# Kernel optimization log

Hardware: AMD Instinct MI355X
Metric: run time of the kernel (lower is better)

Reference implementation:

```python
import jax, jax.numpy as jnp
import numpy as np

B, N, D, C = 256, 256, 512, 1024
EPS = 1e-12  # F.normalize eps


def _l2norm(x):
    n = jnp.linalg.norm(x, axis=-1, keepdims=True)
    return x / jnp.maximum(n, EPS)


def setup_inputs() -> dict:
    key = jax.random.key(0)
    k1, k2, k3 = jax.random.split(key, 3)
    return {
        "image_tokens": jax.random.normal(k1, (B, N, D), dtype=jnp.float32),
        "text_features": jax.random.normal(k2, (C, D), dtype=jnp.float32),
        "log_tau": jnp.asarray(np.log(0.07), dtype=jnp.float32),
        "log_attn_tau": jnp.asarray(np.log(0.07), dtype=jnp.float32),
        "pid_labels": jax.random.randint(k3, (B,), 0, C),
    }


def reference(image_tokens, text_features, log_tau, log_attn_tau, pid_labels):
    toks = _l2norm(image_tokens.astype(jnp.float32))        # [B,N,D]
    txt = _l2norm(text_features.astype(jnp.float32))        # [C,D]
    sims = jnp.einsum('bnd,cd->bnc', toks, txt)             # [B,N,C]
    gt = pid_labels.astype(jnp.int32)
    # sims[arange(B), :, gt] -> [B,N]
    sims_gt = jnp.take_along_axis(sims, gt[:, None, None], axis=2)[..., 0]
    attn_tau = jnp.clip(jnp.exp(log_attn_tau), 0.01, 1.0)
    w = jax.nn.softmax(sims_gt / attn_tau, axis=1)          # [B,N]
    logits = jnp.einsum('bn,bnc->bc', w, sims)              # [B,C]
    tau = jnp.clip(jnp.exp(log_tau), 0.01, 1.0)
    logits = logits / tau
    # cross_entropy with label_smoothing=0.0, mean reduction
    logp = jax.nn.log_softmax(logits, axis=-1)
    nll = -jnp.take_along_axis(logp, gt[:, None], axis=1)[:, 0]
    return jnp.mean(nll)
```

## Files before the change

kernel.cpp:

```cpp
#include <hip/hip_runtime.h>
#include <math.h>

#define Bb 256
#define Nn 256
#define Dd 512
#define Cc 1024
#define KC 8
#define KD (Dd / KC)
#define BT 8

__device__ __forceinline__ float waveReduceSum(float v) {
    #pragma unroll
    for (int off = 32; off > 0; off >>= 1)
        v += __shfl_xor(v, off, 64);
    return v;
}
__device__ __forceinline__ float waveReduceMax(float v) {
    #pragma unroll
    for (int off = 32; off > 0; off >>= 1)
        v = fmaxf(v, __shfl_xor(v, off, 64));
    return v;
}

__global__ void k_txt_prep(const float* __restrict__ txt, float* __restrict__ txt_t) {
    __shared__ float ssp[32][8];
    __shared__ float inv[32];
    __shared__ float tile[32][33];
    const int c0 = blockIdx.x * 32;
    const int t = threadIdx.x;
    {
        const int r = t >> 3, seg = t & 7;
        const float4* p = (const float4*)(txt + (size_t)(c0 + r) * Dd + seg * 64);
        float s = 0.f;
        #pragma unroll
        for (int i = 0; i < 16; ++i) {
            const float4 a = p[i];
            s += a.x*a.x + a.y*a.y + a.z*a.z + a.w*a.w;
        }
        ssp[r][seg] = s;
    }
    __syncthreads();
    if (t < 32) {
        float s = 0.f;
        #pragma unroll
        for (int j = 0; j < 8; ++j) s += ssp[t][j];
        inv[t] = 1.0f / fmaxf(sqrtf(s), 1e-12f);
    }
    __syncthreads();
    const int dx = t & 31, r4 = t >> 5;
    const int dt0 = blockIdx.y * 128;
    for (int dt = dt0; dt < dt0 + 128; dt += 32) {
        #pragma unroll
        for (int rr = r4; rr < 32; rr += 8)
            tile[rr][dx] = txt[(size_t)(c0 + rr) * Dd + dt + dx] * inv[rr];
        __syncthreads();
        #pragma unroll
        for (int rr = r4; rr < 32; rr += 8)
            txt_t[(size_t)(dt + rr) * Cc + c0 + dx] = tile[dx][rr];
        __syncthreads();
    }
}

__global__ void __launch_bounds__(1024) k_attn_q(const float* __restrict__ toks,
                                                 const float* __restrict__ txt,
                                                 const int* __restrict__ pid,
                                                 const float* __restrict__ log_attn_tau,
                                                 float* __restrict__ q) {
    const int b = blockIdx.x;
    const int tid = threadIdx.x;
    const int wv = tid >> 6;
    const int lane = tid & 63;
    __shared__ float xg[Dd];
    __shared__ float r8[8];
    __shared__ float qpart_s[16][Dd];
    __shared__ float ms[16], Ss[16];

    const int g = pid[b];
    float v = 0.f;
    if (tid < Dd) v = txt[(size_t)g * Dd + tid];
    float p = v * v;
    p = waveReduceSum(p);
    if (lane == 0 && wv < 8) r8[wv] = p;
    __syncthreads();
    const float tot = r8[0]+r8[1]+r8[2]+r8[3]+r8[4]+r8[5]+r8[6]+r8[7];
    const float invg = 1.0f / fmaxf(sqrtf(tot), 1e-12f);
    if (tid < Dd) xg[tid] = v * invg;
    __syncthreads();

    float at = expf(log_attn_tau[0]);
    at = fminf(fmaxf(at, 0.01f), 1.0f);
    const float iat = 1.0f / at;

    const float4 xg0 = *(const float4*)&xg[lane * 8];
    const float4 xg1 = *(const float4*)&xg[lane * 8 + 4];

    float m = -INFINITY, S = 0.0f;
    float qa[8] = {0.f, 0.f, 0.f, 0.f, 0.f, 0.f, 0.f, 0.f};

    const float* base = toks + ((size_t)b * Nn + wv * 16) * Dd + (size_t)lane * 8;
    float4 c0[4], c1[4];
    #pragma unroll
    for (int k = 0; k < 4; ++k) {
        c0[k] = *(const float4*)(base + k * Dd);
        c1[k] = *(const float4*)(base + k * Dd + 4);
    }
    #pragma unroll
    for (int batch = 0; batch < 4; ++batch) {
        float4 n0[4], n1[4];
        if (batch < 3) {
            const float* pn = base + (batch + 1) * 4 * Dd;
            #pragma unroll
            for (int k = 0; k < 4; ++k) {
                n0[k] = *(const float4*)(pn + k * Dd);
                n1[k] = *(const float4*)(pn + k * Dd + 4);
            }
        }
        float dt[4], ss[4];
        #pragma unroll
        for (int k = 0; k < 4; ++k) {
            dt[k] = c0[k].x*xg0.x + c0[k].y*xg0.y + c0[k].z*xg0.z + c0[k].w*xg0.w
                  + c1[k].x*xg1.x + c1[k].y*xg1.y + c1[k].z*xg1.z + c1[k].w*xg1.w;
            ss[k] = c0[k].x*c0[k].x + c0[k].y*c0[k].y + c0[k].z*c0[k].z + c0[k].w*c0[k].w
                  + c1[k].x*c1[k].x + c1[k].y*c1[k].y + c1[k].z*c1[k].z + c1[k].w*c1[k].w;
        }
        #pragma unroll
        for (int off = 32; off > 0; off >>= 1) {
            #pragma unroll
            for (int k = 0; k < 4; ++k) {
                dt[k] += __shfl_xor(dt[k], off, 64);
                ss[k] += __shfl_xor(ss[k], off, 64);
            }
        }
        #pragma unroll
        for (int k = 0; k < 4; ++k) {
            const float inv = 1.0f / fmaxf(sqrtf(ss[k]), 1e-12f);
            const float s = dt[k] * inv;
            if (s > m) {
                const float sc = expf((m - s) * iat);
                S = S * sc + 1.0f;
                qa[0] = qa[0]*sc + inv*c0[k].x; qa[1] = qa[1]*sc + inv*c0[k].y;
                qa[2] = qa[2]*sc + inv*c0[k].z; qa[3] = qa[3]*sc + inv*c0[k].w;
                qa[4] = qa[4]*sc + inv*c1[k].x; qa[5] = qa[5]*sc + inv*c1[k].y;
                qa[6] = qa[6]*sc + inv*c1[k].z; qa[7] = qa[7]*sc + inv*c1[k].w;
                m = s;
            } else {
                const float e = expf((s - m) * iat);
                S += e;
                const float w = e * inv;
                qa[0] = fmaf(w, c0[k].x, qa[0]); qa[1] = fmaf(w, c0[k].y, qa[1]);
                qa[2] = fmaf(w, c0[k].z, qa[2]); qa[3] = fmaf(w, c0[k].w, qa[3]);
                qa[4] = fmaf(w, c1[k].x, qa[4]); qa[5] = fmaf(w, c1[k].y, qa[5]);
                qa[6] = fmaf(w, c1[k].z, qa[6]); qa[7] = fmaf(w, c1[k].w, qa[7]);
            }
        }
        #pragma unroll
        for (int k = 0; k < 4; ++k) { c0[k] = n0[k]; c1[k] = n1[k]; }
    }
    #pragma unroll
    for (int j = 0; j < 8; ++j) qpart_s[wv][lane * 8 + j] = qa[j];
    if (lane == 0) { ms[wv] = m; Ss[wv] = S; }
    __syncthreads();
    if (tid < Dd) {
        float M = -INFINITY;
        #pragma unroll
        for (int w = 0; w < 16; ++w) M = fmaxf(M, ms[w]);
        float Stot = 0.f, acc = 0.f;
        #pragma unroll
        for (int w = 0; w < 16; ++w) {
            const float sc = expf((ms[w] - M) * iat);
            Stot = fmaf(Ss[w], sc, Stot);
            acc = fmaf(qpart_s[w][tid], sc, acc);
        }
        q[(size_t)b * Dd + tid] = acc / Stot;
    }
}

__global__ void k_logits(const float* __restrict__ q, const float* __restrict__ txt_t,
                         float* __restrict__ part) {
    const int b0 = blockIdx.x * BT;
    const int kc = blockIdx.y;
    const int d0 = kc * KD;
    const int t = threadIdx.x;
    __shared__ float qs[BT][KD];
    for (int i = t; i < BT * KD; i += 256)
        qs[i >> 6][i & 63] = q[(size_t)(b0 + (i >> 6)) * Dd + d0 + (i & 63)];
    __syncthreads();
    const float4* xt = (const float4*)txt_t;
    float4 a[BT];
    #pragma unroll
    for (int j = 0; j < BT; ++j) a[j] = make_float4(0.f, 0.f, 0.f, 0.f);
    #pragma unroll 2
    for (int d = 0; d < KD; d += 4) {
        const float4 x0 = xt[(size_t)(d0 + d + 0) * (Cc / 4) + t];
        const float4 x1 = xt[(size_t)(d0 + d + 1) * (Cc / 4) + t];
        const float4 x2 = xt[(size_t)(d0 + d + 2) * (Cc / 4) + t];
        const float4 x3 = xt[(size_t)(d0 + d + 3) * (Cc / 4) + t];
        #pragma unroll
        for (int j = 0; j < BT; ++j) {
            const float4 qj = *(const float4*)&qs[j][d];
            a[j].x = fmaf(qj.x,x0.x,a[j].x); a[j].y = fmaf(qj.x,x0.y,a[j].y); a[j].z = fmaf(qj.x,x0.z,a[j].z); a[j].w = fmaf(qj.x,x0.w,a[j].w);
            a[j].x = fmaf(qj.y,x1.x,a[j].x); a[j].y = fmaf(qj.y,x1.y,a[j].y); a[j].z = fmaf(qj.y,x1.z,a[j].z); a[j].w = fmaf(qj.y,x1.w,a[j].w);
            a[j].x = fmaf(qj.z,x2.x,a[j].x); a[j].y = fmaf(qj.z,x2.y,a[j].y); a[j].z = fmaf(qj.z,x2.z,a[j].z); a[j].w = fmaf(qj.z,x2.w,a[j].w);
            a[j].x = fmaf(qj.w,x3.x,a[j].x); a[j].y = fmaf(qj.w,x3.y,a[j].y); a[j].z = fmaf(qj.w,x3.z,a[j].z); a[j].w = fmaf(qj.w,x3.w,a[j].w);
        }
    }
    float* pb = part + ((size_t)kc * Bb + b0) * Cc;
    #pragma unroll
    for (int j = 0; j < BT; ++j) ((float4*)(pb + (size_t)j * Cc))[t] = a[j];
}

__global__ void k_lse(const float* __restrict__ part, const int* __restrict__ pid,
                      const float* __restrict__ log_tau, float* __restrict__ nll) {
    const int b = blockIdx.x;
    const int t = threadIdx.x;
    float4 l = {0,0,0,0};
    #pragma unroll
    for (int kc = 0; kc < KC; ++kc) {
        const float4 p = ((const float4*)(part + ((size_t)kc * Bb + b) * Cc))[t];
        l.x += p.x; l.y += p.y; l.z += p.z; l.w += p.w;
    }
    float tau = expf(log_tau[0]);
    tau = fminf(fmaxf(tau, 0.01f), 1.0f);
    const float itau = 1.0f / tau;
    l.x *= itau; l.y *= itau; l.z *= itau; l.w *= itau;

    const int g = pid[b];
    __shared__ float redm[4], reds[4], sgt;
    if ((g >> 2) == t) {
        const float v[4] = {l.x, l.y, l.z, l.w};
        sgt = v[g & 3];
    }
    float m = fmaxf(fmaxf(l.x, l.y), fmaxf(l.z, l.w));
    m = waveReduceMax(m);
    if ((t & 63) == 0) redm[t >> 6] = m;
    __syncthreads();
    m = fmaxf(fmaxf(redm[0], redm[1]), fmaxf(redm[2], redm[3]));
    float e = expf(l.x - m) + expf(l.y - m) + expf(l.z - m) + expf(l.w - m);
    e = waveReduceSum(e);
    if ((t & 63) == 0) reds[t >> 6] = e;
    __syncthreads();
    if (t == 0) {
        const float S = reds[0] + reds[1] + reds[2] + reds[3];
        nll[b] = m + logf(S) - sgt;
    }
}

__global__ void k_mean(const float* __restrict__ nll, float* __restrict__ out) {
    float v = nll[threadIdx.x];
    __shared__ float red[4];
    v = waveReduceSum(v);
    if ((threadIdx.x & 63) == 0) red[threadIdx.x >> 6] = v;
    __syncthreads();
    if (threadIdx.x == 0) out[0] = (red[0] + red[1] + red[2] + red[3]) * (1.0f / (float)Bb);
}

extern "C" void kernel_launch(void* const* d_in, const int* in_sizes, int n_in,
                              void* d_out, int out_size, void* d_ws, size_t ws_size,
                              hipStream_t stream) {
    const float* toks = (const float*)d_in[0];
    const float* txt = (const float*)d_in[1];
    const float* log_tau = (const float*)d_in[2];
    const float* log_attn_tau = (const float*)d_in[3];
    const int* pid = (const int*)d_in[4];
    float* out = (float*)d_out;

    float* ws = (float*)d_ws;
    float* txt_t = ws;
    float* q     = txt_t + (size_t)Dd * Cc;
    float* part  = q + (size_t)Bb * Dd;
    float* nll   = part + (size_t)KC * Bb * Cc;

    k_txt_prep<<<dim3(Cc / 32, Dd / 128), 256, 0, stream>>>(txt, txt_t);
    k_attn_q<<<Bb, 1024, 0, stream>>>(toks, txt, pid, log_attn_tau, q);
    k_logits<<<dim3(Bb / BT, KC), 256, 0, stream>>>(q, txt_t, part);
    k_lse<<<Bb, 256, 0, stream>>>(part, pid, log_tau, nll);
    k_mean<<<1, 256, 0, stream>>>(nll, out);
}
```

Measured before the change: 219.6 us.

## Fuse text normalization into attention kernel and merge LSE with mean via atomics

Text-feature normalization and transpose move into k_attn_q: each of the 256 blocks normalizes and transposes 4 text rows, which removes the separate k_txt_prep launch. k_lse and k_mean merge into one kernel that accumulates each sample's scaled NLL with atomicAdd, and the last block, found through an atomic counter, writes the result. This saves two kernel launches. In exchange, the transposed stores are uncoalesced, the float sum order becomes nondeterministic, and the accumulators are zeroed inside k_attn_q with a cross-kernel ordering assumption.

New measurement: 220.9 us. No clear change (+0.6%).

```diff
diff --git a/kernel.cpp b/kernel.cpp
--- a/kernel.cpp
+++ b/kernel.cpp
@@ -22,69 +22,50 @@
     return v;
 }
 
-__global__ void k_txt_prep(const float* __restrict__ txt, float* __restrict__ txt_t) {
-    __shared__ float ssp[32][8];
-    __shared__ float inv[32];
-    __shared__ float tile[32][33];
-    const int c0 = blockIdx.x * 32;
-    const int t = threadIdx.x;
-    {
-        const int r = t >> 3, seg = t & 7;
-        const float4* p = (const float4*)(txt + (size_t)(c0 + r) * Dd + seg * 64);
-        float s = 0.f;
-        #pragma unroll
-        for (int i = 0; i < 16; ++i) {
-            const float4 a = p[i];
-            s += a.x*a.x + a.y*a.y + a.z*a.z + a.w*a.w;
-        }
-        ssp[r][seg] = s;
-    }
-    __syncthreads();
-    if (t < 32) {
-        float s = 0.f;
-        #pragma unroll
-        for (int j = 0; j < 8; ++j) s += ssp[t][j];
-        inv[t] = 1.0f / fmaxf(sqrtf(s), 1e-12f);
-    }
-    __syncthreads();
-    const int dx = t & 31, r4 = t >> 5;
-    const int dt0 = blockIdx.y * 128;
-    for (int dt = dt0; dt < dt0 + 128; dt += 32) {
-        #pragma unroll
-        for (int rr = r4; rr < 32; rr += 8)
-            tile[rr][dx] = txt[(size_t)(c0 + rr) * Dd + dt + dx] * inv[rr];
-        __syncthreads();
-        #pragma unroll
-        for (int rr = r4; rr < 32; rr += 8)
-            txt_t[(size_t)(dt + rr) * Cc + c0 + dx] = tile[dx][rr];
-        __syncthreads();
-    }
-}
-
 __global__ void __launch_bounds__(1024) k_attn_q(const float* __restrict__ toks,
                                                  const float* __restrict__ txt,
                                                  const int* __restrict__ pid,
                                                  const float* __restrict__ log_attn_tau,
-                                                 float* __restrict__ q) {
+                                                 float* __restrict__ q,
+                                                 float* __restrict__ txt_t,
+                                                 float* __restrict__ accf,
+                                                 int* __restrict__ cnt) {
     const int b = blockIdx.x;
     const int tid = threadIdx.x;
     const int wv = tid >> 6;
     const int lane = tid & 63;
     __shared__ float xg[Dd];
     __shared__ float r8[8];
+    __shared__ float tss[16];
     __shared__ float qpart_s[16][Dd];
     __shared__ float ms[16], Ss[16];
+
+    if (b == 0 && tid == 0) { accf[0] = 0.0f; cnt[0] = 0; }
 
     const int g = pid[b];
     float v = 0.f;
     if (tid < Dd) v = txt[(size_t)g * Dd + tid];
-    float p = v * v;
-    p = waveReduceSum(p);
-    if (lane == 0 && wv < 8) r8[wv] = p;
-    __syncthreads();
+
+    const int c0 = b * 4;
+    const int row = tid >> 8;
+    const int col2 = (tid & 255) * 2;
+    const float2 tv = *(const float2*)&txt[(size_t)(c0 + row) * Dd + col2];
+
+    float p = waveReduceSum(v * v);
+    float ssp = waveReduceSum(tv.x * tv.x + tv.y * tv.y);
+    if (lane == 0) { if (wv < 8) r8[wv] = p; tss[wv] = ssp; }
+    __syncthreads();
+
     const float tot = r8[0]+r8[1]+r8[2]+r8[3]+r8[4]+r8[5]+r8[6]+r8[7];
     const float invg = 1.0f / fmaxf(sqrtf(tot), 1e-12f);
     if (tid < Dd) xg[tid] = v * invg;
+
+    {
+        const float rss = tss[4*row] + tss[4*row+1] + tss[4*row+2] + tss[4*row+3];
+        const float invr = 1.0f / fmaxf(sqrtf(rss), 1e-12f);
+        txt_t[(size_t)col2 * Cc + c0 + row] = tv.x * invr;
+        txt_t[(size_t)(col2 + 1) * Cc + c0 + row] = tv.y * invr;
+    }
     __syncthreads();
 
     float at = expf(log_attn_tau[0]);
@@ -98,11 +79,11 @@
     float qa[8] = {0.f, 0.f, 0.f, 0.f, 0.f, 0.f, 0.f, 0.f};
 
     const float* base = toks + ((size_t)b * Nn + wv * 16) * Dd + (size_t)lane * 8;
-    float4 c0[4], c1[4];
+    float4 c0v[4], c1v[4];
     #pragma unroll
     for (int k = 0; k < 4; ++k) {
-        c0[k] = *(const float4*)(base + k * Dd);
-        c1[k] = *(const float4*)(base + k * Dd + 4);
+        c0v[k] = *(const float4*)(base + k * Dd);
+        c1v[k] = *(const float4*)(base + k * Dd + 4);
     }
     #pragma unroll
     for (int batch = 0; batch < 4; ++batch) {
@@ -118,10 +99,10 @@
         float dt[4], ss[4];
         #pragma unroll
         for (int k = 0; k < 4; ++k) {
-            dt[k] = c0[k].x*xg0.x + c0[k].y*xg0.y + c0[k].z*xg0.z + c0[k].w*xg0.w
-                  + c1[k].x*xg1.x + c1[k].y*xg1.y + c1[k].z*xg1.z + c1[k].w*xg1.w;
-            ss[k] = c0[k].x*c0[k].x + c0[k].y*c0[k].y + c0[k].z*c0[k].z + c0[k].w*c0[k].w
-                  + c1[k].x*c1[k].x + c1[k].y*c1[k].y + c1[k].z*c1[k].z + c1[k].w*c1[k].w;
+            dt[k] = c0v[k].x*xg0.x + c0v[k].y*xg0.y + c0v[k].z*xg0.z + c0v[k].w*xg0.w
+                  + c1v[k].x*xg1.x + c1v[k].y*xg1.y + c1v[k].z*xg1.z + c1v[k].w*xg1.w;
+            ss[k] = c0v[k].x*c0v[k].x + c0v[k].y*c0v[k].y + c0v[k].z*c0v[k].z + c0v[k].w*c0v[k].w
+                  + c1v[k].x*c1v[k].x + c1v[k].y*c1v[k].y + c1v[k].z*c1v[k].z + c1v[k].w*c1v[k].w;
         }
         #pragma unroll
         for (int off = 32; off > 0; off >>= 1) {
@@ -138,23 +119,23 @@
             if (s > m) {
                 const float sc = expf((m - s) * iat);
                 S = S * sc + 1.0f;
-                qa[0] = qa[0]*sc + inv*c0[k].x; qa[1] = qa[1]*sc + inv*c0[k].y;
-                qa[2] = qa[2]*sc + inv*c0[k].z; qa[3] = qa[3]*sc + inv*c0[k].w;
-                qa[4] = qa[4]*sc + inv*c1[k].x; qa[5] = qa[5]*sc + inv*c1[k].y;
-                qa[6] = qa[6]*sc + inv*c1[k].z; qa[7] = qa[7]*sc + inv*c1[k].w;
+                qa[0] = qa[0]*sc + inv*c0v[k].x; qa[1] = qa[1]*sc + inv*c0v[k].y;
+                qa[2] = qa[2]*sc + inv*c0v[k].z; qa[3] = qa[3]*sc + inv*c0v[k].w;
+                qa[4] = qa[4]*sc + inv*c1v[k].x; qa[5] = qa[5]*sc + inv*c1v[k].y;
+                qa[6] = qa[6]*sc + inv*c1v[k].z; qa[7] = qa[7]*sc + inv*c1v[k].w;
                 m = s;
             } else {
                 const float e = expf((s - m) * iat);
                 S += e;
                 const float w = e * inv;
-                qa[0] = fmaf(w, c0[k].x, qa[0]); qa[1] = fmaf(w, c0[k].y, qa[1]);
-                qa[2] = fmaf(w, c0[k].z, qa[2]); qa[3] = fmaf(w, c0[k].w, qa[3]);
-                qa[4] = fmaf(w, c1[k].x, qa[4]); qa[5] = fmaf(w, c1[k].y, qa[5]);
-                qa[6] = fmaf(w, c1[k].z, qa[6]); qa[7] = fmaf(w, c1[k].w, qa[7]);
+                qa[0] = fmaf(w, c0v[k].x, qa[0]); qa[1] = fmaf(w, c0v[k].y, qa[1]);
+                qa[2] = fmaf(w, c0v[k].z, qa[2]); qa[3] = fmaf(w, c0v[k].w, qa[3]);
+                qa[4] = fmaf(w, c1v[k].x, qa[4]); qa[5] = fmaf(w, c1v[k].y, qa[5]);
+                qa[6] = fmaf(w, c1v[k].z, qa[6]); qa[7] = fmaf(w, c1v[k].w, qa[7]);
             }
         }
         #pragma unroll
-        for (int k = 0; k < 4; ++k) { c0[k] = n0[k]; c1[k] = n1[k]; }
+        for (int k = 0; k < 4; ++k) { c0v[k] = n0[k]; c1v[k] = n1[k]; }
     }
     #pragma unroll
     for (int j = 0; j < 8; ++j) qpart_s[wv][lane * 8 + j] = qa[j];
@@ -209,8 +190,10 @@
     for (int j = 0; j < BT; ++j) ((float4*)(pb + (size_t)j * Cc))[t] = a[j];
 }
 
-__global__ void k_lse(const float* __restrict__ part, const int* __restrict__ pid,
-                      const float* __restrict__ log_tau, float* __restrict__ nll) {
+__global__ void k_lse_mean(const float* __restrict__ part, const int* __restrict__ pid,
+                           const float* __restrict__ log_tau,
+                           float* __restrict__ accf, int* __restrict__ cnt,
+                           float* __restrict__ out) {
     const int b = blockIdx.x;
     const int t = threadIdx.x;
     float4 l = {0,0,0,0};
@@ -241,17 +224,14 @@
     __syncthreads();
     if (t == 0) {
         const float S = reds[0] + reds[1] + reds[2] + reds[3];
-        nll[b] = m + logf(S) - sgt;
-    }
-}
-
-__global__ void k_mean(const float* __restrict__ nll, float* __restrict__ out) {
-    float v = nll[threadIdx.x];
-    __shared__ float red[4];
-    v = waveReduceSum(v);
-    if ((threadIdx.x & 63) == 0) red[threadIdx.x >> 6] = v;
-    __syncthreads();
-    if (threadIdx.x == 0) out[0] = (red[0] + red[1] + red[2] + red[3]) * (1.0f / (float)Bb);
+        const float my = (m + logf(S) - sgt) * (1.0f / (float)Bb);
+        atomicAdd(accf, my);
+        __threadfence();
+        const int c = atomicAdd(cnt, 1);
+        if (c == Bb - 1) {
+            out[0] = atomicAdd(accf, 0.0f);
+        }
+    }
 }
 
 extern "C" void kernel_launch(void* const* d_in, const int* in_sizes, int n_in,
@@ -268,11 +248,10 @@
     float* txt_t = ws;
     float* q     = txt_t + (size_t)Dd * Cc;
     float* part  = q + (size_t)Bb * Dd;
-    float* nll   = part + (size_t)KC * Bb * Cc;
-
-    k_txt_prep<<<dim3(Cc / 32, Dd / 128), 256, 0, stream>>>(txt, txt_t);
-    k_attn_q<<<Bb, 1024, 0, stream>>>(toks, txt, pid, log_attn_tau, q);
+    float* accf  = part + (size_t)KC * Bb * Cc;
+    int*   cnt   = (int*)(accf + 1);
+
+    k_attn_q<<<Bb, 1024, 0, stream>>>(toks, txt, pid, log_attn_tau, q, txt_t, accf, cnt);
     k_logits<<<dim3(Bb / BT, KC), 256, 0, stream>>>(q, txt_t, part);
-    k_lse<<<Bb, 256, 0, stream>>>(part, pid, log_tau, nll);
-    k_mean<<<1, 256, 0, stream>>>(nll, out);
-}
+    k_lse_mean<<<Bb, 256, 0, stream>>>(part, pid, log_tau, accf, cnt, out);
+}
```
